# Kernel tuning notes

Measured on AMD Instinct MI355X. Metric: run time of the kernel, lower is better.

Reference implementation:

```python
import jax, jax.numpy as jnp
import numpy as np

N = 50000        # nodes
F = 128          # input feature dim
U = 128          # units (output dim)
E_RAND = 1_600_000  # random edges; N self-loops appended -> E = 1_650_000
LABEL_IDXS = np.array([0, 5, 17, 42], dtype=np.int32)  # label_idxs init arg (indices into F)


def setup_inputs() -> dict:
    key = jax.random.key(0)
    k1, k2, k3, k4, k5 = jax.random.split(key, 5)
    x = jax.random.normal(k1, (1, N, F), dtype=jnp.float32)
    src = jax.random.randint(k2, (E_RAND,), 0, N, dtype=jnp.int32)
    dst = jax.random.randint(k3, (E_RAND,), 0, N, dtype=jnp.int32)
    # append self-loops so the diagonal of A (Adiag term) is nontrivial,
    # matching a normalized Laplacian which always has diagonal entries
    loops = jnp.arange(N, dtype=jnp.int32)
    edge_src = jnp.concatenate([src, loops])
    edge_dst = jnp.concatenate([dst, loops])
    edge_w = jax.random.uniform(k4, (E_RAND + N,), dtype=jnp.float32)
    kernel = jax.random.normal(k5, (F, U), dtype=jnp.float32) * (1.0 / np.sqrt(F))
    bias = jnp.zeros((U,), dtype=jnp.float32)
    return {"x": x, "edge_src": edge_src, "edge_dst": edge_dst,
            "edge_w": edge_w, "kernel": kernel, "bias": bias}


def reference(x, edge_src, edge_dst, edge_w, kernel, bias):
    # x: [1, N, F]; sparse A given as COO edges (edge_src=row i, edge_dst=col j, edge_w=A[i,j])
    n = x.shape[1]
    xs = x[0]  # [N, F]
    # A @ X  (sparse matmul via gather + segment_sum)
    agg = jax.ops.segment_sum(edge_w[:, None] * xs[edge_dst], edge_src, num_segments=n)  # [N, F]
    # diag(A): entries where row == col
    diag = jax.ops.segment_sum(jnp.where(edge_src == edge_dst, edge_w, jnp.float32(0.0)),
                               edge_src, num_segments=n)  # [N]
    # B = sum_{i in label_idxs} e_i e_i^T is a diagonal 0/1 selector on feature columns,
    # so (Adiag @ X) @ B == diag[:,None] * (X * mask)
    mask = jnp.zeros((xs.shape[1],), xs.dtype).at[jnp.asarray(LABEL_IDXS)].set(1.0)  # [F]
    h = agg - diag[:, None] * (xs * mask)  # [N, F]
    out = jax.nn.relu(h @ kernel + bias)   # [N, U]
    return out[None]  # [1, N, U]
```

## Files before the change

### kernel.cpp

```cpp
#include <hip/hip_runtime.h>

#define FDIM 128
#define UDIM 128
#define BROWS 32
#define CAP   1408
#define TILE  4096
#define EPT   16
#define NPAIR 4

typedef __attribute__((ext_vector_type(8))) short short8;
typedef __attribute__((ext_vector_type(4))) float floatx4;
typedef __attribute__((ext_vector_type(2))) float f32x2;

__device__ inline unsigned int round_bf16_bits(float a) {
  unsigned int ua = __float_as_uint(a);
  ua += 0x7fffu + ((ua >> 16) & 1u);
  return ua & 0xffff0000u;
}
__device__ inline unsigned int pack_bf16(float a, float b) {
  unsigned int ua = __float_as_uint(a);
  unsigned int ub = __float_as_uint(b);
  ua += 0x7fffu + ((ua >> 16) & 1u);
  ub += 0x7fffu + ((ub >> 16) & 1u);
  return (ua >> 16) | (ub & 0xffff0000u);
}

__global__ __launch_bounds__(256) void prep(
    const float* __restrict__ K, uint4* __restrict__ kfrag,
    int* __restrict__ zbase, int zcount) {
  int gid = blockIdx.x * 256 + threadIdx.x;
  if (gid < 2048) {
    int lane = gid & 63, bb = gid >> 6;
    int n = (bb >> 2) * 16 + (lane & 15);
    int k0 = (bb & 3) * 32 + (lane >> 4) * 8;
    unsigned int pq[4];
    #pragma unroll
    for (int j = 0; j < 4; ++j) {
      float a = K[(size_t)(k0 + 2 * j) * UDIM + n];
      float b = K[(size_t)(k0 + 2 * j + 1) * UDIM + n];
      pq[j] = pack_bf16(a, b);
    }
    kfrag[gid] = make_uint4(pq[0], pq[1], pq[2], pq[3]);
  }
  if (gid < zcount) zbase[gid] = 0;
}

__device__ void bin_dev(int blk, const int* __restrict__ src,
                        const int* __restrict__ dst, const float* __restrict__ w,
                        int* __restrict__ cursor, uint2* __restrict__ meta,
                        float* __restrict__ diag, int E, int NB, char* smem) {
  int* scnt  = (int*)smem;
  int* sbase = scnt + NB;
  int* scur  = sbase + NB;
  int t = threadIdx.x;
  for (int b = t; b < NB; b += 256) { scnt[b] = 0; scur[b] = 0; }
  __syncthreads();

  uint2 pay[EPT];
  int e0 = blk * TILE;
  #pragma unroll
  for (int j = 0; j < EPT; ++j) {
    int e = e0 + j * 256 + t;
    if (e < E) {
      int s = src[e];
      int d = dst[e];
      float wv = w[e];
      if (s == d) atomicAdd(&diag[s], wv);
      pay[j].x = round_bf16_bits(wv) | (unsigned int)d;
      pay[j].y = (unsigned int)s;
      atomicAdd(&scnt[s >> 5], 1);
    } else {
      pay[j].y = 0xffffffffu;
    }
  }
  __syncthreads();

  for (int b = t; b < NB; b += 256) {
    int c = scnt[b];
    if (c) sbase[b] = b * CAP + atomicAdd(&cursor[b], c);
  }
  __syncthreads();

  #pragma unroll
  for (int j = 0; j < EPT; ++j) {
    if (pay[j].y != 0xffffffffu) {
      int b = (int)(pay[j].y >> 5);
      int r = atomicAdd(&scur[b], 1);
      int pos = sbase[b] + r;
      if (pos < (b + 1) * CAP)
        meta[pos] = make_uint2(pay[j].x, pay[j].y & 31u);
    }
  }
}

__device__ void gemm_dev(int g, const float* __restrict__ x,
                         const uint4* __restrict__ kfrag,
                         unsigned short* __restrict__ Ybf, int N, char* smem) {
  unsigned short (*sX)[136] = (unsigned short (*)[136])smem;
  int t = threadIdx.x;
  int r0 = g * 64;

  #pragma unroll
  for (int i = 0; i < 8; ++i) {
    int li = i * 256 + t;
    int row = li >> 5;
    int col4 = (li & 31) * 4;
    int gr = r0 + row; if (gr > N - 1) gr = N - 1;
    float4 v = *(const float4*)(x + (size_t)gr * FDIM + col4);
    *(uint2*)(&sX[row][col4]) = make_uint2(pack_bf16(v.x, v.y), pack_bf16(v.z, v.w));
  }
  __syncthreads();

  int wave = t >> 6, lane = t & 63;
  int m = lane & 15, q = lane >> 4;

  short8 bf[2][4];
  #pragma unroll
  for (int c = 0; c < 2; ++c)
    #pragma unroll
    for (int ks = 0; ks < 4; ++ks)
      bf[c][ks] = *(const short8*)&kfrag[(size_t)((2 * wave + c) * 4 + ks) * 64 + lane];

  floatx4 acc[4][2];
  #pragma unroll
  for (int rt = 0; rt < 4; ++rt)
    #pragma unroll
    for (int c = 0; c < 2; ++c)
      acc[rt][c] = (floatx4){0.f, 0.f, 0.f, 0.f};

  #pragma unroll
  for (int ks = 0; ks < 4; ++ks) {
    #pragma unroll
    for (int rt = 0; rt < 4; ++rt) {
      short8 af = *(const short8*)&sX[rt * 16 + m][ks * 32 + q * 8];
      acc[rt][0] = __builtin_amdgcn_mfma_f32_16x16x32_bf16(af, bf[0][ks], acc[rt][0], 0, 0, 0);
      acc[rt][1] = __builtin_amdgcn_mfma_f32_16x16x32_bf16(af, bf[1][ks], acc[rt][1], 0, 0, 0);
    }
  }

  unsigned short* yp = Ybf + (size_t)wave * N * 32;
  #pragma unroll
  for (int rt = 0; rt < 4; ++rt) {
    #pragma unroll
    for (int c = 0; c < 2; ++c) {
      int off = c * 16 + m;
      #pragma unroll
      for (int reg = 0; reg < 4; ++reg) {
        int r = r0 + rt * 16 + q * 4 + reg;
        if (r < N)
          yp[(size_t)r * 32 + off] =
              (unsigned short)(round_bf16_bits(acc[rt][c][reg]) >> 16);
      }
    }
  }
}

__global__ __launch_bounds__(256) void bin_gemm(
    const int* __restrict__ src, const int* __restrict__ dst,
    const float* __restrict__ w, int* __restrict__ cursor,
    uint2* __restrict__ meta, float* __restrict__ diag,
    const float* __restrict__ x, const uint4* __restrict__ kfrag,
    unsigned short* __restrict__ Ybf, int N, int E, int NB, int nbin) {
  __shared__ alignas(16) char smem[18816];
  if (blockIdx.x < (unsigned)nbin)
    bin_dev(blockIdx.x, src, dst, w, cursor, meta, diag, E, NB, smem);
  else
    gemm_dev(blockIdx.x - nbin, x, kfrag, Ybf, N, smem);
}

__global__ __launch_bounds__(256) void sortk(
    const uint2* __restrict__ meta, const int* __restrict__ cursor,
    unsigned int* __restrict__ sortedg, int* __restrict__ rstartg,
    int* __restrict__ permg,
    const float* __restrict__ diag, const float* __restrict__ x,
    float4* __restrict__ dscaleg, int N) {
  __shared__ unsigned int sdstw[CAP];
  __shared__ unsigned int sorted[CAP];
  __shared__ unsigned char skey[CAP];
  __shared__ int kcnt[BROWS];
  __shared__ int rstart[BROWS + 1];
  int b = blockIdx.x;
  int t = threadIdx.x;
  int cntE = cursor[b]; if (cntE > CAP) cntE = CAP;
  const uint2* mb = meta + (size_t)b * CAP;

  if (t < BROWS) {
    kcnt[t] = 0;
    int g = b * BROWS + t;
    if (g < N) {
      float dg = diag[g];
      dscaleg[g] = make_float4(dg * x[(size_t)g * FDIM + 0],
                               dg * x[(size_t)g * FDIM + 5],
                               dg * x[(size_t)g * FDIM + 17],
                               dg * x[(size_t)g * FDIM + 42]);
    }
  }
  __syncthreads();

  for (int e = t; e < cntE; e += 256) {
    uint2 m = mb[e];
    sdstw[e] = m.x;
    skey[e] = (unsigned char)m.y;
    atomicAdd(&kcnt[m.y & 31u], 1);
  }
  __syncthreads();

  if (t < 64) {
    int v = (t < BROWS) ? kcnt[t] : 0;
    if (t < BROWS) {
      int incl = v;
      #pragma unroll
      for (int off = 1; off < BROWS; off <<= 1) {
        int u = __shfl_up(incl, off, 64);
        if (t >= off) incl += u;
      }
      rstart[t + 1] = incl;
      kcnt[t] = incl - v;
      if (t == 0) rstart[0] = 0;
    }
    int lane = t;
    int key = (t < BROWS) ? ((v << 6) | t) : -1;
    #pragma unroll
    for (int k = 2; k <= 32; k <<= 1) {
      #pragma unroll
      for (int j = k >> 1; j > 0; j >>= 1) {
        int other = __shfl_xor(key, j, 64);
        bool up = ((lane & k) == 0);
        bool takeBig = ((lane & j) == 0);
        bool keep = up ? (takeBig ? key >= other : key <= other)
                       : (takeBig ? key <= other : key >= other);
        key = keep ? key : other;
      }
    }
    if (t < BROWS) permg[b * BROWS + t] = key & 63;
  }
  __syncthreads();

  for (int e = t; e < cntE; e += 256) {
    int k = skey[e];
    int pos = atomicAdd(&kcnt[k], 1);
    sorted[pos] = sdstw[e];
  }
  __syncthreads();

  unsigned int* sg = sortedg + (size_t)b * CAP;
  for (int e = t; e < cntE; e += 256) sg[e] = sorted[e];
  if (t < BROWS + 1) rstartg[b * (BROWS + 1) + t] = rstart[t];
}

__global__ __launch_bounds__(256, 8) void gather_slab(
    const unsigned short* __restrict__ Ybf, const unsigned int* __restrict__ sortedg,
    const int* __restrict__ rstartg, const int* __restrict__ permg,
    const float4* __restrict__ dscaleg,
    const float* __restrict__ K, const float* __restrict__ bias,
    float* __restrict__ out, int N) {
  __shared__ alignas(16) unsigned int srow[CAP];
  __shared__ int rsl[BROWS + 1];
  __shared__ int sperm[BROWS];
  __shared__ float4 dsc[BROWS];
  int bi = blockIdx.x;
  int p = bi & 3;
  int b = bi >> 2;
  int t = threadIdx.x;
  int lane = t & 63, wave = t >> 6;
  int rs = lane >> 3;
  int fp = lane & 7;

  if (t < BROWS + 1) rsl[t] = rstartg[b * (BROWS + 1) + t];
  if (t < BROWS) {
    sperm[t] = permg[b * BROWS + t];
    int gg = b * BROWS + t;
    dsc[t] = (gg < N) ? dscaleg[gg] : make_float4(0.f, 0.f, 0.f, 0.f);
  }
  __syncthreads();
  int cnt = rsl[BROWS];

  const unsigned int* sg = sortedg + (size_t)b * CAP;
  int nc4 = cnt >> 2;
  for (int i = t; i < nc4; i += 256)
    ((uint4*)srow)[i] = ((const uint4*)sg)[i];
  for (int e = nc4 * 4 + t; e < cnt; e += 256) srow[e] = sg[e];
  __syncthreads();

  int r = sperm[wave * 8 + rs];
  int g = b * BROWS + r;
  const unsigned short* yp = Ybf + (size_t)p * N * 32;
  int base = rsl[r];
  int len = rsl[r + 1] - base;

  int ml = len;
  ml = max(ml, __shfl_xor(ml, 8, 64));
  ml = max(ml, __shfl_xor(ml, 16, 64));
  ml = max(ml, __shfl_xor(ml, 32, 64));

  f32x2 acc01 = {0.f, 0.f}, acc23 = {0.f, 0.f};
  for (int k = 0; k < ml; k += 2) {
    bool v0 = (k < len), v1 = (k + 1 < len);
    unsigned int w0 = srow[v0 ? base + k : 0];
    unsigned int w1 = srow[v1 ? base + k + 1 : 0];
    w0 = v0 ? w0 : 0u;
    w1 = v1 ? w1 : 0u;
    uint2 pk0 = *(const uint2*)(yp + (size_t)(w0 & 0xffffu) * 32 + fp * 4);
    uint2 pk1 = *(const uint2*)(yp + (size_t)(w1 & 0xffffu) * 32 + fp * 4);
    float wj0 = __uint_as_float(w0 & 0xffff0000u);
    float wj1 = __uint_as_float(w1 & 0xffff0000u);
    f32x2 wv0 = {wj0, wj0}, wv1 = {wj1, wj1};
    f32x2 a0 = {__uint_as_float(pk0.x << 16), __uint_as_float(pk0.x & 0xffff0000u)};
    f32x2 a1 = {__uint_as_float(pk0.y << 16), __uint_as_float(pk0.y & 0xffff0000u)};
    f32x2 b0 = {__uint_as_float(pk1.x << 16), __uint_as_float(pk1.x & 0xffff0000u)};
    f32x2 b1 = {__uint_as_float(pk1.y << 16), __uint_as_float(pk1.y & 0xffff0000u)};
    acc01 += wv0 * a0;
    acc23 += wv0 * a1;
    acc01 += wv1 * b0;
    acc23 += wv1 * b1;
  }

  if (g < N) {
    float4 acc = make_float4(acc01[0], acc01[1], acc23[0], acc23[1]);
    float4 ds = dsc[r];
    const int lf[4] = {0, 5, 17, 42};
    float dsv[4] = {ds.x, ds.y, ds.z, ds.w};
    #pragma unroll
    for (int tt = 0; tt < 4; ++tt) {
      float4 k4 = *(const float4*)(K + (size_t)lf[tt] * UDIM + p * 32 + fp * 4);
      acc.x -= dsv[tt] * k4.x; acc.y -= dsv[tt] * k4.y;
      acc.z -= dsv[tt] * k4.z; acc.w -= dsv[tt] * k4.w;
    }
    float4 b4 = *(const float4*)(bias + p * 32 + fp * 4);
    acc.x = fmaxf(acc.x + b4.x, 0.f);
    acc.y = fmaxf(acc.y + b4.y, 0.f);
    acc.z = fmaxf(acc.z + b4.z, 0.f);
    acc.w = fmaxf(acc.w + b4.w, 0.f);
    *(float4*)(out + (size_t)g * UDIM + p * 32 + fp * 4) = acc;
  }
}

extern "C" void kernel_launch(void* const* d_in, const int* in_sizes, int n_in,
                              void* d_out, int out_size, void* d_ws, size_t ws_size,
                              hipStream_t stream) {
  const float* x    = (const float*)d_in[0];
  const int*   esrc = (const int*)d_in[1];
  const int*   edst = (const int*)d_in[2];
  const float* ew   = (const float*)d_in[3];
  const float* K    = (const float*)d_in[4];
  const float* bias = (const float*)d_in[5];
  float* out = (float*)d_out;

  const int N = in_sizes[0] / FDIM;
  const int E = in_sizes[1];
  const int NB = (N + BROWS - 1) / BROWS;

  char* p = (char*)d_ws;
  unsigned short* Ybf = (unsigned short*)p; p += (size_t)N * UDIM * 2;
  float* diag  = (float*)p;         p += (size_t)N * 4;
  int*   cursor = (int*)p;          p += (size_t)NB * 4;
  uint4* kfrag = (uint4*)p;         p += (size_t)32 * 64 * 16;
  uint2* meta = (uint2*)p;          p += (size_t)NB * CAP * 8;
  unsigned int* sortedg = (unsigned int*)p; p += (size_t)NB * CAP * 4;
  int* rstartg = (int*)p;           p += (size_t)NB * (BROWS + 2) * 4;
  int* permg = (int*)p;             p += (size_t)NB * BROWS * 4;
  p = (char*)(((uintptr_t)p + 15) & ~(uintptr_t)15);
  float4* dscaleg = (float4*)p;     p += (size_t)N * 16;

  const int nbin = (E + TILE - 1) / TILE;
  const int ngemm = (N + 63) / 64;

  prep<<<(N + NB + 255) / 256, 256, 0, stream>>>(K, kfrag, (int*)diag, N + NB);
  bin_gemm<<<nbin + ngemm, 256, 0, stream>>>(
      esrc, edst, ew, cursor, meta, diag, x, kfrag, Ybf, N, E, NB, nbin);
  sortk<<<NB, 256, 0, stream>>>(meta, cursor, sortedg, rstartg, permg,
                                diag, x, dscaleg, N);
  gather_slab<<<NB * NPAIR, 256, 0, stream>>>(
      Ybf, sortedg, rstartg, permg, dscaleg, K, bias, out, N);
}
```

Before: 175.7 us.

## Replace global atomic bin cursors with per-tile local sort and offset tables

The binning stage no longer reserves space in per-bucket global regions through atomics on a shared cursor array. Each edge tile now sorts its edges by bucket in shared memory, writes them out contiguously, and stores a per-tile table of bucket offsets. The sort kernel then reads, for its bucket, the segment from every tile, using a prefix scan over tile lengths to place them. This removes global atomic contention and scattered 8-byte writes, at the cost of each sort block reading NT offset pairs and doing many small serial per-tile copies, plus a large NT×NB offset table.

```diff
diff --git a/kernel.cpp b/kernel.cpp
--- a/kernel.cpp
+++ b/kernel.cpp
@@ -7,6 +7,7 @@
 #define TILE  4096
 #define EPT   16
 #define NPAIR 4
+#define NTMAX 512
 
 typedef __attribute__((ext_vector_type(8))) short short8;
 typedef __attribute__((ext_vector_type(4))) float floatx4;
@@ -23,6 +24,40 @@
   ua += 0x7fffu + ((ua >> 16) & 1u);
   ub += 0x7fffu + ((ub >> 16) & 1u);
   return (ua >> 16) | (ub & 0xffff0000u);
+}
+
+__device__ void block_scan_excl(int* A, int n, int* tpart, int* wtot) {
+  int t = threadIdx.x;
+  int per = (n + 255) >> 8;
+  int s0 = t * per;
+  int local = 0;
+  for (int k = 0; k < per; ++k) {
+    int i = s0 + k;
+    if (i < n) local += A[i];
+  }
+  tpart[t] = local;
+  __syncthreads();
+  int lane = t & 63, w = t >> 6;
+  int v = tpart[t];
+  int incl = v;
+  #pragma unroll
+  for (int off = 1; off < 64; off <<= 1) {
+    int u = __shfl_up(incl, off, 64);
+    if (lane >= off) incl += u;
+  }
+  if (lane == 63) wtot[w] = incl;
+  __syncthreads();
+  int woff = 0;
+  #pragma unroll
+  for (int i = 0; i < 4; ++i) woff += (i < w) ? wtot[i] : 0;
+  int excl = woff + incl - v;
+  int run = excl;
+  for (int k = 0; k < per; ++k) {
+    int i = s0 + k;
+    if (i < n) { int a = A[i]; A[i] = run; run += a; }
+  }
+  if (t == 255) A[n] = run;
+  __syncthreads();
 }
 
 __global__ __launch_bounds__(256) void prep(
@@ -47,13 +82,18 @@
 
 __device__ void bin_dev(int blk, const int* __restrict__ src,
                         const int* __restrict__ dst, const float* __restrict__ w,
-                        int* __restrict__ cursor, uint2* __restrict__ meta,
-                        float* __restrict__ diag, int E, int NB, char* smem) {
+                        unsigned int* __restrict__ sorted4g,
+                        unsigned char* __restrict__ key5g,
+                        int* __restrict__ sbg, float* __restrict__ diag,
+                        int E, int NB, char* smem) {
   int* scnt  = (int*)smem;
-  int* sbase = scnt + NB;
-  int* scur  = sbase + NB;
+  int* scur  = scnt + (NB + 1);
+  int* tpart = scur + NB;
+  int* wtot  = tpart + 256;
+  unsigned int* sord = (unsigned int*)(wtot + 8);
+  unsigned char* krow = (unsigned char*)(sord + TILE);
   int t = threadIdx.x;
-  for (int b = t; b < NB; b += 256) { scnt[b] = 0; scur[b] = 0; }
+  for (int b = t; b <= NB; b += 256) scnt[b] = 0;
   __syncthreads();
 
   uint2 pay[EPT];
@@ -75,22 +115,31 @@
   }
   __syncthreads();
 
-  for (int b = t; b < NB; b += 256) {
-    int c = scnt[b];
-    if (c) sbase[b] = b * CAP + atomicAdd(&cursor[b], c);
-  }
+  block_scan_excl(scnt, NB, tpart, wtot);
+
+  for (int b = t; b < NB; b += 256) scur[b] = scnt[b];
   __syncthreads();
 
   #pragma unroll
   for (int j = 0; j < EPT; ++j) {
     if (pay[j].y != 0xffffffffu) {
       int b = (int)(pay[j].y >> 5);
-      int r = atomicAdd(&scur[b], 1);
-      int pos = sbase[b] + r;
-      if (pos < (b + 1) * CAP)
-        meta[pos] = make_uint2(pay[j].x, pay[j].y & 31u);
-    }
-  }
+      int pos = atomicAdd(&scur[b], 1);
+      sord[pos] = pay[j].x;
+      krow[pos] = (unsigned char)(pay[j].y & 31u);
+    }
+  }
+  __syncthreads();
+
+  unsigned int* s4 = sorted4g + (size_t)blk * TILE;
+  #pragma unroll
+  for (int i = 0; i < TILE / 256; ++i) s4[i * 256 + t] = sord[i * 256 + t];
+  unsigned int* k4 = (unsigned int*)(key5g + (size_t)blk * TILE);
+  #pragma unroll
+  for (int i = 0; i < TILE / 1024; ++i)
+    k4[i * 256 + t] = ((unsigned int*)krow)[i * 256 + t];
+  int* sb = sbg + (size_t)blk * (NB + 1);
+  for (int b = t; b <= NB; b += 256) sb[b] = scnt[b];
 }
 
 __device__ void gemm_dev(int g, const float* __restrict__ x,
@@ -157,32 +206,35 @@
 
 __global__ __launch_bounds__(256) void bin_gemm(
     const int* __restrict__ src, const int* __restrict__ dst,
-    const float* __restrict__ w, int* __restrict__ cursor,
-    uint2* __restrict__ meta, float* __restrict__ diag,
+    const float* __restrict__ w,
+    unsigned int* __restrict__ sorted4g, unsigned char* __restrict__ key5g,
+    int* __restrict__ sbg, float* __restrict__ diag,
     const float* __restrict__ x, const uint4* __restrict__ kfrag,
     unsigned short* __restrict__ Ybf, int N, int E, int NB, int nbin) {
-  __shared__ alignas(16) char smem[18816];
+  __shared__ alignas(16) char smem[34048];
   if (blockIdx.x < (unsigned)nbin)
-    bin_dev(blockIdx.x, src, dst, w, cursor, meta, diag, E, NB, smem);
+    bin_dev(blockIdx.x, src, dst, w, sorted4g, key5g, sbg, diag, E, NB, smem);
   else
     gemm_dev(blockIdx.x - nbin, x, kfrag, Ybf, N, smem);
 }
 
 __global__ __launch_bounds__(256) void sortk(
-    const uint2* __restrict__ meta, const int* __restrict__ cursor,
+    const unsigned int* __restrict__ sorted4g, const unsigned char* __restrict__ key5g,
+    const int* __restrict__ sbg,
     unsigned int* __restrict__ sortedg, int* __restrict__ rstartg,
     int* __restrict__ permg,
     const float* __restrict__ diag, const float* __restrict__ x,
-    float4* __restrict__ dscaleg, int N) {
+    float4* __restrict__ dscaleg, int N, int NB, int NT) {
   __shared__ unsigned int sdstw[CAP];
   __shared__ unsigned int sorted[CAP];
   __shared__ unsigned char skey[CAP];
   __shared__ int kcnt[BROWS];
   __shared__ int rstart[BROWS + 1];
+  __shared__ int mlen[NTMAX + 1];
+  __shared__ int tpart[256];
+  __shared__ int wtot[8];
   int b = blockIdx.x;
   int t = threadIdx.x;
-  int cntE = cursor[b]; if (cntE > CAP) cntE = CAP;
-  const uint2* mb = meta + (size_t)b * CAP;
 
   if (t < BROWS) {
     kcnt[t] = 0;
@@ -195,13 +247,30 @@
                                dg * x[(size_t)g * FDIM + 42]);
     }
   }
-  __syncthreads();
-
-  for (int e = t; e < cntE; e += 256) {
-    uint2 m = mb[e];
-    sdstw[e] = m.x;
-    skey[e] = (unsigned char)m.y;
-    atomicAdd(&kcnt[m.y & 31u], 1);
+
+  for (int tt = t; tt < NT; tt += 256) {
+    const int* sb = sbg + (size_t)tt * (NB + 1) + b;
+    mlen[tt] = sb[1] - sb[0];
+  }
+  __syncthreads();
+  block_scan_excl(mlen, NT, tpart, wtot);
+  int cntE = mlen[NT]; if (cntE > CAP) cntE = CAP;
+
+  for (int tt = t; tt < NT; tt += 256) {
+    int s0 = sbg[(size_t)tt * (NB + 1) + b];
+    int dofs = mlen[tt];
+    int len = mlen[tt + 1] - mlen[tt];
+    const unsigned int* s4 = sorted4g + (size_t)tt * TILE + s0;
+    const unsigned char* k5 = key5g + (size_t)tt * TILE + s0;
+    for (int k = 0; k < len; ++k) {
+      int pos = dofs + k;
+      if (pos < CAP) {
+        unsigned char ky = k5[k];
+        sdstw[pos] = s4[k];
+        skey[pos] = ky;
+        atomicAdd(&kcnt[ky], 1);
+      }
+    }
   }
   __syncthreads();
 
@@ -349,27 +418,29 @@
   const int N = in_sizes[0] / FDIM;
   const int E = in_sizes[1];
   const int NB = (N + BROWS - 1) / BROWS;
+  const int NT = (E + TILE - 1) / TILE;
 
   char* p = (char*)d_ws;
   unsigned short* Ybf = (unsigned short*)p; p += (size_t)N * UDIM * 2;
   float* diag  = (float*)p;         p += (size_t)N * 4;
-  int*   cursor = (int*)p;          p += (size_t)NB * 4;
   uint4* kfrag = (uint4*)p;         p += (size_t)32 * 64 * 16;
-  uint2* meta = (uint2*)p;          p += (size_t)NB * CAP * 8;
+  unsigned int* sorted4g = (unsigned int*)p; p += (size_t)NT * TILE * 4;
+  unsigned char* key5g = (unsigned char*)p;  p += (size_t)NT * TILE;
+  int* sbg = (int*)p;               p += (size_t)NT * (NB + 1) * 4;
   unsigned int* sortedg = (unsigned int*)p; p += (size_t)NB * CAP * 4;
   int* rstartg = (int*)p;           p += (size_t)NB * (BROWS + 2) * 4;
   int* permg = (int*)p;             p += (size_t)NB * BROWS * 4;
   p = (char*)(((uintptr_t)p + 15) & ~(uintptr_t)15);
   float4* dscaleg = (float4*)p;     p += (size_t)N * 16;
 
-  const int nbin = (E + TILE - 1) / TILE;
+  const int nbin = NT;
   const int ngemm = (N + 63) / 64;
 
-  prep<<<(N + NB + 255) / 256, 256, 0, stream>>>(K, kfrag, (int*)diag, N + NB);
+  prep<<<(N + 255) / 256, 256, 0, stream>>>(K, kfrag, (int*)diag, N);
   bin_gemm<<<nbin + ngemm, 256, 0, stream>>>(
-      esrc, edst, ew, cursor, meta, diag, x, kfrag, Ybf, N, E, NB, nbin);
-  sortk<<<NB, 256, 0, stream>>>(meta, cursor, sortedg, rstartg, permg,
-                                diag, x, dscaleg, N);
+      esrc, edst, ew, sorted4g, key5g, sbg, diag, x, kfrag, Ybf, N, E, NB, nbin);
+  sortk<<<NB, 256, 0, stream>>>(sorted4g, key5g, sbg, sortedg, rstartg, permg,
+                                diag, x, dscaleg, N, NB, NT);
   gather_slab<<<NB * NPAIR, 256, 0, stream>>>(
       Ybf, sortedg, rstartg, permg, dscaleg, K, bias, out, N);
 }
```

After: 189.8 us. +8.0%, slower.
